# Kernel tuning notes

Hardware: AMD Instinct MI355X
Metric: run time of the kernel (lower is better)

## Reference

```python
import jax, jax.numpy as jnp
import numpy as np

BS, M, CLIP_DIM = 64, 1000, 512
D = 512
N_WAYS = 20
N_Z = 8


def setup_inputs() -> dict:
    key = jax.random.key(0)
    ks = jax.random.split(key, 16)
    s = 0.02
    inp = {
        "x_context": jax.random.normal(ks[0], (BS, M, CLIP_DIM), jnp.float32),
        "y_context": jax.random.randint(ks[1], (BS, M), 0, N_WAYS),
        "x_query": jax.random.normal(ks[2], (BS, M, CLIP_DIM), jnp.float32),
        # image_proj
        "Wp": jax.random.normal(ks[3], (CLIP_DIM, D), jnp.float32) * s,
        "bp": jnp.zeros((D,), jnp.float32),
        # aggregator: Linear(d,d) -> GELU -> Linear(d,2d)
        "Wa1": jax.random.normal(ks[4], (D, D), jnp.float32) * s,
        "ba1": jnp.zeros((D,), jnp.float32),
        "Wa2": jax.random.normal(ks[5], (D, 2 * D), jnp.float32) * s,
        "ba2": jnp.zeros((2 * D,), jnp.float32),
        # decoder: Linear(d,d) -> GELU -> Linear(d,d)
        "Wd1": jax.random.normal(ks[6], (D, D), jnp.float32) * s,
        "bd1": jnp.zeros((D,), jnp.float32),
        "Wd2": jax.random.normal(ks[7], (D, D), jnp.float32) * s,
        "bd2": jnp.zeros((D,), jnp.float32),
    }
    return inp


def reference(x_context, y_context, x_query, Wp, bp, Wa1, ba1, Wa2, ba2, Wd1, bd1, Wd2, bd2):
    # project image embeddings: [bs, M, clip_dim] -> [bs, M, d]
    xc = x_context @ Wp + bp
    xq = x_query @ Wp + bp

    # encode_context_per_class: per-class masked sum == one-hot segment-sum
    # (original loops over classes doing (x*mask).sum(dim=1))
    oh = jax.nn.one_hot(y_context, N_WAYS, dtype=xc.dtype)  # [bs, M, N]
    r_C = jnp.einsum('bmn,bmd->bnd', oh, xc)  # [bs, N, d]

    # knowledge is None -> k = zeros; combined = relu(r + 0)
    combined = jax.nn.relu(r_C)
    h = jax.nn.gelu(combined @ Wa1 + ba1, approximate=False)
    stats = h @ Wa2 + ba2  # [bs, N, 2d]
    mu, scale_raw = stats[..., :D], stats[..., D:]
    scale = 0.01 + 0.99 * jax.nn.softplus(scale_raw)

    # eval path: sample n_z from q(z|C) via reparameterization
    eps = jax.random.normal(jax.random.key(42), (N_Z,) + mu.shape, mu.dtype)
    z_samples = mu[None] + scale[None] * eps  # [n_z, bs, N, d]

    # decode: class weight vectors then inner product with queries
    W = jax.nn.gelu(z_samples @ Wd1 + bd1, approximate=False) @ Wd2 + bd2
    logits = jnp.einsum('bqd,sbnd->sbqn', xq, W)  # [n_z, bs, Q*N, N]
    return logits, z_samples, mu, scale
```

## Files before the change

kernel.cpp:

```cpp
#include <hip/hip_runtime.h>
#include <hip/hip_bf16.h>
#include <stdint.h>


typedef __attribute__((ext_vector_type(8))) short short8;
typedef __attribute__((ext_vector_type(4))) float f32x4;

__device__ __forceinline__ float gelu_f(float x) {
    return 0.5f * x * (1.0f + erff(x * 0.70710678118654752440f));
}
__device__ __forceinline__ float softplus_f(float x) {
    return fmaxf(x, 0.0f) + log1pf(expf(-fabsf(x)));
}
__device__ __forceinline__ uint32_t cvt2(float a, float b) {
    __hip_bfloat162 h;
    h.x = __float2bfloat16(a);
    h.y = __float2bfloat16(b);
    uint32_t u; __builtin_memcpy(&u, &h, 4); return u;
}
__device__ __forceinline__ unsigned short f2bfu(float f) {
    __hip_bfloat16 h = __float2bfloat16(f);
    unsigned short u; __builtin_memcpy(&u, &h, 2); return u;
}
__device__ __forceinline__ float bfu2f(unsigned short u) {
    uint32_t v = (uint32_t)u << 16; float f; __builtin_memcpy(&f, &v, 4); return f;
}

__device__ __forceinline__ void threefry2x32(uint32_t k0, uint32_t k1,
                                             uint32_t x0, uint32_t x1,
                                             uint32_t& o0, uint32_t& o1) {
    uint32_t ks[3] = {k0, k1, k0 ^ k1 ^ 0x1BD11BDAu};
    x0 += ks[0]; x1 += ks[1];
    const uint32_t rot[8] = {13,15,26,6,17,29,16,24};
#pragma unroll
    for (int i = 0; i < 5; i++) {
#pragma unroll
        for (int j = 0; j < 4; j++) {
            uint32_t r = rot[(i & 1) * 4 + j];
            x0 += x1;
            x1 = (x1 << r) | (x1 >> (32 - r));
            x1 ^= x0;
        }
        x0 += ks[(i + 1) % 3];
        x1 += ks[(i + 2) % 3] + (uint32_t)(i + 1);
    }
    o0 = x0; o1 = x1;
}

__device__ __forceinline__ float bits_to_normal(uint32_t b) {
    float f = __uint_as_float((b >> 9) | 0x3F800000u) - 1.0f;
    const float lo = __uint_as_float(0xBF7FFFFFu);
    float u = fmaxf(lo, f * 2.0f + lo);
    return 1.41421356237309504880f * erfinvf(u);
}

__global__ __launch_bounds__(512) void scatter_k(const float* __restrict__ xc,
                                                 const int* __restrict__ y,
                                                 float* __restrict__ Apart,
                                                 float* __restrict__ cntpart) {
    __shared__ float sA[20 * 512];
    __shared__ float scnt[20];
    const int b = blockIdx.x, ch = blockIdx.y;
    const int tid = threadIdx.x;
    for (int i = tid; i < 20 * 512; i += 512) sA[i] = 0.f;
    if (tid < 20) scnt[tid] = 0.f;
    __syncthreads();
    const int m0 = ch * 125;
    const size_t xbase = ((size_t)b * 1000 + m0) * 512 + tid;
    const int ybase = b * 1000 + m0;

    float xv[8]; int cv[8];
#pragma unroll
    for (int j = 0; j < 8; j++) {
        xv[j] = xc[xbase + (size_t)j * 512];
        cv[j] = y[ybase + j];
    }
    int p = 8;
    for (int pan = 0; pan < 15; pan++) {
        float xn[8]; int cn[8];
        const bool more = (pan < 14);
        if (more) {
#pragma unroll
            for (int j = 0; j < 8; j++) {
                xn[j] = xc[xbase + (size_t)(p + j) * 512];
                cn[j] = y[ybase + p + j];
            }
        }
#pragma unroll
        for (int j = 0; j < 8; j++) {
            sA[cv[j] * 512 + tid] += xv[j];
            if (tid == 0) scnt[cv[j]] += 1.f;
        }
        if (more) {
#pragma unroll
            for (int j = 0; j < 8; j++) { xv[j] = xn[j]; cv[j] = cn[j]; }
            p += 8;
        }
    }
#pragma unroll
    for (int j = 0; j < 5; j++) {
        float xx = xc[xbase + (size_t)(120 + j) * 512];
        int cc = y[ybase + 120 + j];
        sA[cc * 512 + tid] += xx;
        if (tid == 0) scnt[cc] += 1.f;
    }
    __syncthreads();
    float* dst = Apart + (size_t)ch * 655360 + (size_t)b * 10240;
    for (int i = tid; i < 10240; i += 512) dst[i] = sA[i];
    if (tid < 20) cntpart[(size_t)ch * 1280 + b * 20 + tid] = scnt[tid];
}

__global__ __launch_bounds__(256) void reduce_bf_k(const float* __restrict__ Apart,
                                                   const float* __restrict__ cntpart,
                                                   unsigned short* __restrict__ Abf,
                                                   float* __restrict__ cnt) {
    int i = blockIdx.x * 256 + threadIdx.x;
    if (i < 163840) {
        const float4* Ap4 = (const float4*)Apart;
        float4 s = Ap4[i];
#pragma unroll
        for (int p = 1; p < 8; p++) {
            float4 v = Ap4[(size_t)p * 163840 + i];
            s.x += v.x; s.y += v.y; s.z += v.z; s.w += v.w;
        }
        uint2 o;
        o.x = cvt2(s.x, s.y); o.y = cvt2(s.z, s.w);
        *(uint2*)&Abf[(size_t)i * 4] = o;
    }
    if (i < 1280) {
        float s = 0.f;
#pragma unroll
        for (int p = 0; p < 8; p++) s += cntpart[p * 1280 + i];
        cnt[i] = s;
    }
}

__global__ __launch_bounds__(256) void wtg_k(const float* __restrict__ src,
                                             unsigned short* __restrict__ dst,
                                             int R, int C) {
    __shared__ float T[64][65];
    const int r0 = blockIdx.y * 64, c0 = blockIdx.x * 64;
    const int tid = threadIdx.x;
    const int rr = tid >> 4, cc = (tid & 15) * 4;
#pragma unroll
    for (int l = 0; l < 4; l++) {
        int row = rr + l * 16;
        float4 v = *(const float4*)&src[(size_t)(r0 + row) * C + c0 + cc];
        T[row][cc] = v.x; T[row][cc+1] = v.y; T[row][cc+2] = v.z; T[row][cc+3] = v.w;
    }
    __syncthreads();
#pragma unroll
    for (int l = 0; l < 4; l++) {
        int n = rr + l * 16;
        uint2 u;
        u.x = cvt2(T[cc][n], T[cc+1][n]);
        u.y = cvt2(T[cc+2][n], T[cc+3][n]);
        *(uint2*)&dst[(size_t)(c0 + n) * R + r0 + cc] = u;
    }
}

__global__ __launch_bounds__(256) void wconv_k(const float* __restrict__ in,
                                               unsigned short* __restrict__ o, int n2) {
    int i = blockIdx.x * 256 + threadIdx.x;
    if (i < n2) {
        float2 v = *(const float2*)&in[i * 2];
        *(uint32_t*)&o[i * 2] = cvt2(v.x, v.y);
    }
}

template <int EPI>
__global__ __launch_bounds__(256) void gm2_k(const unsigned short* __restrict__ Abf,
                                             const unsigned short* __restrict__ Bbf,
                                             const float* __restrict__ bias,
                                             const float* __restrict__ extra,
                                             unsigned short* __restrict__ C0,
                                             float* __restrict__ F0,
                                             float* __restrict__ F1,
                                             int Nn) {
    __shared__ unsigned short As[64 * 64];
    __shared__ unsigned short Bs[128 * 64];
    const int tid = threadIdx.x;
    const int lane = tid & 63, w = tid >> 6;
    const int row0 = blockIdx.y * 64, col0 = blockIdx.x * 128;
    f32x4 acc[4][2] = {};
    for (int k0 = 0; k0 < 512; k0 += 64) {
        {
            int row = tid >> 2, cs = (tid & 3) * 16;
            int swz = (row & 7) << 4;
            const unsigned short* src = Abf + (size_t)(row0 + row) * 512 + k0 + cs;
#pragma unroll
            for (int j = 0; j < 2; j++) {
                uint4 u = *(const uint4*)(src + j * 8);
                *(uint4*)((char*)As + row * 128 + (((cs + j * 8) * 2) ^ swz)) = u;
            }
        }
        {
            int row = tid >> 1, cs = (tid & 1) * 32;
            int swz = (row & 7) << 4;
            const unsigned short* src = Bbf + (size_t)(col0 + row) * 512 + k0 + cs;
#pragma unroll
            for (int j = 0; j < 4; j++) {
                uint4 u = *(const uint4*)(src + j * 8);
                *(uint4*)((char*)Bs + row * 128 + (((cs + j * 8) * 2) ^ swz)) = u;
            }
        }
        __syncthreads();
#pragma unroll
        for (int ks = 0; ks < 2; ks++) {
            short8 a[4], bb[2];
#pragma unroll
            for (int mi = 0; mi < 4; mi++) {
                int r = mi * 16 + (lane & 15);
                a[mi] = *(const short8*)((const char*)As + r * 128 +
                          (((ks * 32 + (lane >> 4) * 8) * 2) ^ ((r & 7) << 4)));
            }
#pragma unroll
            for (int ni = 0; ni < 2; ni++) {
                int n = w * 32 + ni * 16 + (lane & 15);
                bb[ni] = *(const short8*)((const char*)Bs + n * 128 +
                          (((ks * 32 + (lane >> 4) * 8) * 2) ^ ((n & 7) << 4)));
            }
#pragma unroll
            for (int mi = 0; mi < 4; mi++)
#pragma unroll
                for (int ni = 0; ni < 2; ni++)
                    acc[mi][ni] = __builtin_amdgcn_mfma_f32_16x16x32_bf16(a[mi], bb[ni], acc[mi][ni], 0, 0, 0);
        }
        __syncthreads();
    }
#pragma unroll
    for (int mi = 0; mi < 4; mi++) {
#pragma unroll
        for (int ni = 0; ni < 2; ni++) {
            int c = col0 + w * 32 + ni * 16 + (lane & 15);
            float bv = bias ? bias[c] : 0.f;
#pragma unroll
            for (int j = 0; j < 4; j++) {
                int r = row0 + mi * 16 + (lane >> 4) * 4 + j;
                float v = acc[mi][ni][j];
                if (EPI == 0) {
                    v += bv;
                    C0[(size_t)r * Nn + c] = f2bfu(v);
                } else if (EPI == 1) {
                    v += extra[r] * bv;
                    C0[(size_t)r * Nn + c] = f2bfu(fmaxf(v, 0.f));
                } else if (EPI == 2) {
                    C0[(size_t)r * Nn + c] = f2bfu(gelu_f(v + bv));
                } else {
                    v += bv;
                    if (c < 512) F0[(size_t)r * 512 + c] = v;
                    else F1[(size_t)r * 512 + (c - 512)] = 0.01f + 0.99f * softplus_f(v);
                }
            }
        }
    }
}

__global__ __launch_bounds__(256) void z2_k(const float* __restrict__ mu,
                                            const float* __restrict__ sc,
                                            float* __restrict__ z,
                                            unsigned short* __restrict__ zb) {
    const uint32_t NH = 2621440u;
    uint32_t i = blockIdx.x * 256u + threadIdx.x;
    if (i >= NH) return;
    uint32_t t0 = 2u * i;
    uint32_t o0, o1, p0, p1;
    threefry2x32(0u, 42u, 0u, t0, o0, o1);
    threefry2x32(0u, 42u, 0u, t0 + 1u, p0, p1);
    uint32_t r0 = t0 % 655360u;
    float2 mv = *(const float2*)&mu[r0];
    float2 sv = *(const float2*)&sc[r0];
    float z0 = mv.x + sv.x * bits_to_normal(o0 ^ o1);
    float z1 = mv.y + sv.y * bits_to_normal(p0 ^ p1);
    float2 zo; zo.x = z0; zo.y = z1;
    *(float2*)&z[t0] = zo;
    *(uint32_t*)&zb[t0] = cvt2(z0, z1);
}

__global__ __launch_bounds__(256) void beta_bf_k(const unsigned short* __restrict__ Wfb,
                                                 const float* __restrict__ bp,
                                                 float* __restrict__ beta) {
    int wave = threadIdx.x >> 6, lane = threadIdx.x & 63;
    int r = blockIdx.x * 4 + wave;
    short8 wv = *(const short8*)(Wfb + (size_t)r * 512 + lane * 8);
    float s = 0.f;
#pragma unroll
    for (int e = 0; e < 8; e++) s += bp[lane * 8 + e] * bfu2f((unsigned short)wv[e]);
#pragma unroll
    for (int o = 32; o > 0; o >>= 1) s += __shfl_down(s, o, 64);
    if (lane == 0) beta[r] = s;
}

__global__ __launch_bounds__(512) void logits_mfma3_k(const float* __restrict__ Xq,
                                                      const unsigned short* __restrict__ Vb,
                                                      const float* __restrict__ beta,
                                                      float* __restrict__ out) {
    __shared__ unsigned short Vs[160 * 64];
    __shared__ float bs[160];
    const int u = blockIdx.x + 8 * blockIdx.y;
    const int xcd = u & 7, idx = u >> 3;
    const int b = (idx & 7) * 8 + xcd;
    const int qh = idx >> 3;
    const int tid = threadIdx.x, lane = tid & 63, w = tid >> 6;
    const int wq = w >> 1, wn = w & 1;

    if (tid < 160) {
        int s = tid / 20, n = tid - s * 20;
        bs[tid] = beta[(size_t)(s * 64 + b) * 20 + n];
    }

    const int klane = (lane >> 4) * 8;
    const float* xp[2];
    int qb[2];
#pragma unroll
    for (int qs = 0; qs < 2; qs++) {
        qb[qs] = qh * 128 + wq * 32 + qs * 16;
        int qr = qb[qs] + (lane & 15);
        if (qr > 999) qr = 999;
        xp[qs] = Xq + ((size_t)b * 1000 + qr) * 512 + klane;
    }
    int vrow[5], vswz[5];
#pragma unroll
    for (int nf = 0; nf < 5; nf++) {
        int rr = wn * 80 + nf * 16 + (lane & 15);
        vrow[nf] = rr * 128;
        vswz[nf] = (rr & 7) << 4;
    }

    f32x4 acc[2][5] = {};
    for (int k0 = 0; k0 < 512; k0 += 64) {
        __syncthreads();
        for (int c = tid; c < 640; c += 512) {
            int row = c >> 2, off = (c & 3) * 32;
            int sdiv = row / 20;
            int row_g = row + sdiv * 1260 + b * 20;
            const unsigned short* src = Vb + (size_t)row_g * 512 + k0 + (c & 3) * 16;
            uint4 u0 = *(const uint4*)src;
            uint4 u1 = *(const uint4*)(src + 8);
            int swz = (row & 7) << 4;
            char* base = (char*)Vs + row * 128;
            *(uint4*)(base + (off ^ swz)) = u0;
            *(uint4*)(base + ((off + 16) ^ swz)) = u1;
        }
        __syncthreads();
#pragma unroll
        for (int ks = 0; ks < 2; ks++) {
            int kb = (ks * 32 + klane) * 2;
            short8 bf[5];
#pragma unroll
            for (int nf = 0; nf < 5; nf++)
                bf[nf] = *(const short8*)((const char*)Vs + vrow[nf] + (kb ^ vswz[nf]));
            short8 af[2];
#pragma unroll
            for (int qs = 0; qs < 2; qs++) {
                const float* p = xp[qs] + k0 + ks * 32;
                float4 v0 = *(const float4*)p;
                float4 v1 = *(const float4*)(p + 4);
                uint4 uu;
                uu.x = cvt2(v0.x, v0.y); uu.y = cvt2(v0.z, v0.w);
                uu.z = cvt2(v1.x, v1.y); uu.w = cvt2(v1.z, v1.w);
                __builtin_memcpy(&af[qs], &uu, 16);
            }
#pragma unroll
            for (int qs = 0; qs < 2; qs++)
#pragma unroll
                for (int nf = 0; nf < 5; nf++)
                    acc[qs][nf] = __builtin_amdgcn_mfma_f32_16x16x32_bf16(af[qs], bf[nf], acc[qs][nf], 0, 0, 0);
        }
    }

#pragma unroll
    for (int nf = 0; nf < 5; nf++) {
        int rl = wn * 80 + nf * 16 + (lane & 15);
        int s = rl / 20, n = rl - s * 20;
        float bb = bs[rl];
        size_t ob = (size_t)(s * 64 + b) * 20000;
#pragma unroll
        for (int qs = 0; qs < 2; qs++) {
#pragma unroll
            for (int j = 0; j < 4; j++) {
                int q = qb[qs] + (lane >> 4) * 4 + j;
                if (q < 1000)
                    out[ob + (size_t)q * 20 + n] = acc[qs][nf][j] + bb;
            }
        }
    }
}

extern "C" void kernel_launch(void* const* d_in, const int* in_sizes, int n_in,
                              void* d_out, int out_size, void* d_ws, size_t ws_size,
                              hipStream_t stream) {
    const float* x_context = (const float*)d_in[0];
    const int*   y_context = (const int*)d_in[1];
    const float* x_query   = (const float*)d_in[2];
    const float* Wp  = (const float*)d_in[3];
    const float* bp  = (const float*)d_in[4];
    const float* Wa1 = (const float*)d_in[5];
    const float* ba1 = (const float*)d_in[6];
    const float* Wa2 = (const float*)d_in[7];
    const float* ba2 = (const float*)d_in[8];
    const float* Wd1 = (const float*)d_in[9];
    const float* bd1 = (const float*)d_in[10];
    const float* Wd2 = (const float*)d_in[11];
    const float* bd2 = (const float*)d_in[12];

    float* out    = (float*)d_out;
    float* logits = out;
    float* z      = out + 10240000;
    float* mu     = out + 15482880;
    float* sc     = out + 16138240;
    unsigned short* Wfb = (unsigned short*)d_out;

    float* ws   = (float*)d_ws;
    float* cnt  = ws;
    float* beta = cnt + 1280;
    unsigned short* WpTb  = (unsigned short*)(beta + 10240);
    unsigned short* Wa1Tb = WpTb + 262144;
    unsigned short* Wa2Tb = Wa1Tb + 262144;
    unsigned short* WdT1b = Wa2Tb + 524288;
    unsigned short* WdT2b = WdT1b + 262144;
    unsigned short* Wpb   = WdT2b + 262144;
    unsigned short* Abf   = Wpb + 262144;
    unsigned short* combb = Abf + 655360;
    unsigned short* hb    = combb + 655360;
    unsigned short* zb    = hb + 655360;
    unsigned short* Vbf   = zb + 5242880;
    float* big = (float*)(Vbf + 5242880);
    unsigned short* Wgb = (unsigned short*)big;

    wtg_k<<<dim3(8, 8), 256, 0, stream>>>(Wp,  WpTb,  512, 512);
    wtg_k<<<dim3(8, 8), 256, 0, stream>>>(Wa1, Wa1Tb, 512, 512);
    wtg_k<<<dim3(16, 8), 256, 0, stream>>>(Wa2, Wa2Tb, 512, 1024);
    wtg_k<<<dim3(8, 8), 256, 0, stream>>>(Wd1, WdT1b, 512, 512);
    wtg_k<<<dim3(8, 8), 256, 0, stream>>>(Wd2, WdT2b, 512, 512);
    wconv_k<<<dim3(512), 256, 0, stream>>>(Wp, Wpb, 131072);
    scatter_k<<<dim3(64, 8), 512, 0, stream>>>(x_context, y_context, big , beta );
    reduce_bf_k<<<dim3(640), 256, 0, stream>>>(big, beta, Abf, cnt);
    gm2_k<1><<<dim3(4, 20), 256, 0, stream>>>(Abf, WpTb, bp, cnt, combb, nullptr, nullptr, 512);
    gm2_k<2><<<dim3(4, 20), 256, 0, stream>>>(combb, Wa1Tb, ba1, nullptr, hb, nullptr, nullptr, 512);
    gm2_k<3><<<dim3(8, 20), 256, 0, stream>>>(hb, Wa2Tb, ba2, nullptr, nullptr, mu, sc, 1024);
    z2_k<<<dim3(10240), 256, 0, stream>>>(mu, sc, z, zb);
    gm2_k<2><<<dim3(4, 160), 256, 0, stream>>>(zb, WdT1b, bd1, nullptr, Wgb, nullptr, nullptr, 512);
    gm2_k<0><<<dim3(4, 160), 256, 0, stream>>>(Wgb, WdT2b, bd2, nullptr, Wfb, nullptr, nullptr, 512);
    gm2_k<0><<<dim3(4, 160), 256, 0, stream>>>(Wfb, Wpb, nullptr, nullptr, Vbf, nullptr, nullptr, 512);
    beta_bf_k<<<dim3(2560), 256, 0, stream>>>(Wfb, bp, beta);
    logits_mfma3_k<<<dim3(8, 64), 512, 0, stream>>>(x_query, Vbf, beta, logits);
}
```

Baseline: 235.2 us.

## Precompose Wd2 with Wp and fuse weight prep into one kernel

Reassociates the decoder output and image projection by precomputing the product of Wp and Wd2 once as a small GEMM. This removes one large 10240x512x512 GEMM over the sampled weights, and the bias terms are folded into precomputed vectors and a constant. All weight transposes and conversions, the bias dot products and the class counts are merged into a single prep kernel, which cuts launch count; the counts are now computed with shared atomics instead of inside scatter. The composed weight is rounded to bf16, which changes rounding behaviour.

New measurement: 229.4 us. 1.03x faster.

```diff
diff --git a/kernel.cpp b/kernel.cpp
--- a/kernel.cpp
+++ b/kernel.cpp
@@ -54,16 +54,100 @@
     return 1.41421356237309504880f * erfinvf(u);
 }
 
+__global__ __launch_bounds__(256) void prep_k(
+    const float* __restrict__ Wp, const float* __restrict__ Wa1,
+    const float* __restrict__ Wa2, const float* __restrict__ Wd1,
+    const float* __restrict__ Wd2, const float* __restrict__ bp,
+    const float* __restrict__ bd2, const int* __restrict__ y,
+    unsigned short* __restrict__ WpTb, unsigned short* __restrict__ Wa1Tb,
+    unsigned short* __restrict__ Wa2Tb, unsigned short* __restrict__ WdT1b,
+    unsigned short* __restrict__ Wpb, unsigned short* __restrict__ Wd2b,
+    float* __restrict__ bv, float* __restrict__ w2bp,
+    float* __restrict__ c0, float* __restrict__ cnt)
+{
+    __shared__ float T[64][65];
+    __shared__ int lc[32];
+    __shared__ float ws4[4];
+    const int f = blockIdx.x;
+    const int tid = threadIdx.x;
+
+    if (f < 320) {
+        const float* src; unsigned short* dst; int C, t, xb, yb;
+        if (f < 64)       { src = Wp;  dst = WpTb;  C = 512;  t = f;       xb = t & 7;  yb = t >> 3; }
+        else if (f < 128) { src = Wa1; dst = Wa1Tb; C = 512;  t = f - 64;  xb = t & 7;  yb = t >> 3; }
+        else if (f < 256) { src = Wa2; dst = Wa2Tb; C = 1024; t = f - 128; xb = t & 15; yb = t >> 4; }
+        else              { src = Wd1; dst = WdT1b; C = 512;  t = f - 256; xb = t & 7;  yb = t >> 3; }
+        const int r0 = yb * 64, cc0 = xb * 64;
+        const int rr = tid >> 4, cc = (tid & 15) * 4;
+#pragma unroll
+        for (int l = 0; l < 4; l++) {
+            int row = rr + l * 16;
+            float4 v = *(const float4*)&src[(size_t)(r0 + row) * C + cc0 + cc];
+            T[row][cc] = v.x; T[row][cc+1] = v.y; T[row][cc+2] = v.z; T[row][cc+3] = v.w;
+        }
+        __syncthreads();
+#pragma unroll
+        for (int l = 0; l < 4; l++) {
+            int n = rr + l * 16;
+            uint2 u;
+            u.x = cvt2(T[cc][n], T[cc+1][n]);
+            u.y = cvt2(T[cc+2][n], T[cc+3][n]);
+            *(uint2*)&dst[(size_t)(cc0 + n) * 512 + r0 + cc] = u;
+        }
+    } else if (f < 576) {
+        const float* src = (f < 448) ? Wp : Wd2;
+        unsigned short* dst = (f < 448) ? Wpb : Wd2b;
+        int t = (f < 448) ? f - 320 : f - 448;
+        size_t i = ((size_t)t * 256 + tid) * 8;
+        float4 a = *(const float4*)&src[i];
+        float4 b4 = *(const float4*)&src[i + 4];
+        uint4 u;
+        u.x = cvt2(a.x, a.y);  u.y = cvt2(a.z, a.w);
+        u.z = cvt2(b4.x, b4.y); u.w = cvt2(b4.z, b4.w);
+        *(uint4*)&dst[i] = u;
+    } else if (f < 832) {
+        const float* W = (f < 704) ? Wp : Wd2;
+        const float* v = (f < 704) ? bd2 : bp;
+        float* o = (f < 704) ? bv : w2bp;
+        int t = (f < 704) ? f - 576 : f - 704;
+        int wave = tid >> 6, lane = tid & 63;
+        int r = t * 4 + wave;
+        const float* row = W + (size_t)r * 512 + lane * 8;
+        float4 x0 = *(const float4*)row;
+        float4 x1 = *(const float4*)(row + 4);
+        float4 v0 = *(const float4*)&v[lane * 8];
+        float4 v1 = *(const float4*)&v[lane * 8 + 4];
+        float s = x0.x*v0.x + x0.y*v0.y + x0.z*v0.z + x0.w*v0.w
+                + x1.x*v1.x + x1.y*v1.y + x1.z*v1.z + x1.w*v1.w;
+#pragma unroll
+        for (int off = 32; off > 0; off >>= 1) s += __shfl_down(s, off, 64);
+        if (lane == 0) o[r] = s;
+    } else if (f == 832) {
+        float s = bp[tid] * bd2[tid] + bp[tid + 256] * bd2[tid + 256];
+#pragma unroll
+        for (int off = 32; off > 0; off >>= 1) s += __shfl_down(s, off, 64);
+        int wave = tid >> 6, lane = tid & 63;
+        if (lane == 0) ws4[wave] = s;
+        __syncthreads();
+        if (tid == 0) c0[0] = ws4[0] + ws4[1] + ws4[2] + ws4[3];
+    } else {
+        int b = f - 833;
+        if (tid < 32) lc[tid] = 0;
+        __syncthreads();
+        for (int m = tid; m < 1000; m += 256)
+            atomicAdd(&lc[y[b * 1000 + m]], 1);
+        __syncthreads();
+        if (tid < 20) cnt[b * 20 + tid] = (float)lc[tid];
+    }
+}
+
 __global__ __launch_bounds__(512) void scatter_k(const float* __restrict__ xc,
                                                  const int* __restrict__ y,
-                                                 float* __restrict__ Apart,
-                                                 float* __restrict__ cntpart) {
+                                                 float* __restrict__ Apart) {
     __shared__ float sA[20 * 512];
-    __shared__ float scnt[20];
     const int b = blockIdx.x, ch = blockIdx.y;
     const int tid = threadIdx.x;
     for (int i = tid; i < 20 * 512; i += 512) sA[i] = 0.f;
-    if (tid < 20) scnt[tid] = 0.f;
     __syncthreads();
     const int m0 = ch * 125;
     const size_t xbase = ((size_t)b * 1000 + m0) * 512 + tid;
@@ -87,10 +171,7 @@
             }
         }
 #pragma unroll
-        for (int j = 0; j < 8; j++) {
-            sA[cv[j] * 512 + tid] += xv[j];
-            if (tid == 0) scnt[cv[j]] += 1.f;
-        }
+        for (int j = 0; j < 8; j++) sA[cv[j] * 512 + tid] += xv[j];
         if (more) {
 #pragma unroll
             for (int j = 0; j < 8; j++) { xv[j] = xn[j]; cv[j] = cn[j]; }
@@ -102,18 +183,14 @@
         float xx = xc[xbase + (size_t)(120 + j) * 512];
         int cc = y[ybase + 120 + j];
         sA[cc * 512 + tid] += xx;
-        if (tid == 0) scnt[cc] += 1.f;
     }
     __syncthreads();
     float* dst = Apart + (size_t)ch * 655360 + (size_t)b * 10240;
     for (int i = tid; i < 10240; i += 512) dst[i] = sA[i];
-    if (tid < 20) cntpart[(size_t)ch * 1280 + b * 20 + tid] = scnt[tid];
 }
 
 __global__ __launch_bounds__(256) void reduce_bf_k(const float* __restrict__ Apart,
-                                                   const float* __restrict__ cntpart,
-                                                   unsigned short* __restrict__ Abf,
-                                                   float* __restrict__ cnt) {
+                                                   unsigned short* __restrict__ Abf) {
     int i = blockIdx.x * 256 + threadIdx.x;
     if (i < 163840) {
         const float4* Ap4 = (const float4*)Apart;
@@ -126,45 +203,6 @@
         uint2 o;
         o.x = cvt2(s.x, s.y); o.y = cvt2(s.z, s.w);
         *(uint2*)&Abf[(size_t)i * 4] = o;
-    }
-    if (i < 1280) {
-        float s = 0.f;
-#pragma unroll
-        for (int p = 0; p < 8; p++) s += cntpart[p * 1280 + i];
-        cnt[i] = s;
-    }
-}
-
-__global__ __launch_bounds__(256) void wtg_k(const float* __restrict__ src,
-                                             unsigned short* __restrict__ dst,
-                                             int R, int C) {
-    __shared__ float T[64][65];
-    const int r0 = blockIdx.y * 64, c0 = blockIdx.x * 64;
-    const int tid = threadIdx.x;
-    const int rr = tid >> 4, cc = (tid & 15) * 4;
-#pragma unroll
-    for (int l = 0; l < 4; l++) {
-        int row = rr + l * 16;
-        float4 v = *(const float4*)&src[(size_t)(r0 + row) * C + c0 + cc];
-        T[row][cc] = v.x; T[row][cc+1] = v.y; T[row][cc+2] = v.z; T[row][cc+3] = v.w;
-    }
-    __syncthreads();
-#pragma unroll
-    for (int l = 0; l < 4; l++) {
-        int n = rr + l * 16;
-        uint2 u;
-        u.x = cvt2(T[cc][n], T[cc+1][n]);
-        u.y = cvt2(T[cc+2][n], T[cc+3][n]);
-        *(uint2*)&dst[(size_t)(c0 + n) * R + r0 + cc] = u;
-    }
-}
-
-__global__ __launch_bounds__(256) void wconv_k(const float* __restrict__ in,
-                                               unsigned short* __restrict__ o, int n2) {
-    int i = blockIdx.x * 256 + threadIdx.x;
-    if (i < n2) {
-        float2 v = *(const float2*)&in[i * 2];
-        *(uint32_t*)&o[i * 2] = cvt2(v.x, v.y);
     }
 }
 
@@ -277,18 +315,19 @@
     *(uint32_t*)&zb[t0] = cvt2(z0, z1);
 }
 
-__global__ __launch_bounds__(256) void beta_bf_k(const unsigned short* __restrict__ Wfb,
-                                                 const float* __restrict__ bp,
-                                                 float* __restrict__ beta) {
+__global__ __launch_bounds__(256) void beta2_k(const unsigned short* __restrict__ Wgb,
+                                               const float* __restrict__ vec,
+                                               const float* __restrict__ c0,
+                                               float* __restrict__ beta) {
     int wave = threadIdx.x >> 6, lane = threadIdx.x & 63;
     int r = blockIdx.x * 4 + wave;
-    short8 wv = *(const short8*)(Wfb + (size_t)r * 512 + lane * 8);
+    short8 wv = *(const short8*)(Wgb + (size_t)r * 512 + lane * 8);
     float s = 0.f;
 #pragma unroll
-    for (int e = 0; e < 8; e++) s += bp[lane * 8 + e] * bfu2f((unsigned short)wv[e]);
+    for (int e = 0; e < 8; e++) s += vec[lane * 8 + e] * bfu2f((unsigned short)wv[e]);
 #pragma unroll
     for (int o = 32; o > 0; o >>= 1) s += __shfl_down(s, o, 64);
-    if (lane == 0) beta[r] = s;
+    if (lane == 0) beta[r] = s + c0[0];
 }
 
 __global__ __launch_bounds__(512) void logits_mfma3_k(const float* __restrict__ Xq,
@@ -409,18 +448,21 @@
     float* z      = out + 10240000;
     float* mu     = out + 15482880;
     float* sc     = out + 16138240;
-    unsigned short* Wfb = (unsigned short*)d_out;
 
     float* ws   = (float*)d_ws;
     float* cnt  = ws;
     float* beta = cnt + 1280;
-    unsigned short* WpTb  = (unsigned short*)(beta + 10240);
+    float* bv   = beta + 10240;
+    float* w2bp = bv + 512;
+    float* c0   = w2bp + 512;
+    unsigned short* WpTb  = (unsigned short*)(c0 + 63);
     unsigned short* Wa1Tb = WpTb + 262144;
     unsigned short* Wa2Tb = Wa1Tb + 262144;
     unsigned short* WdT1b = Wa2Tb + 524288;
-    unsigned short* WdT2b = WdT1b + 262144;
-    unsigned short* Wpb   = WdT2b + 262144;
-    unsigned short* Abf   = Wpb + 262144;
+    unsigned short* Wpb   = WdT1b + 262144;
+    unsigned short* Wd2b  = Wpb + 262144;
+    unsigned short* Gtb   = Wd2b + 262144;
+    unsigned short* Abf   = Gtb + 262144;
     unsigned short* combb = Abf + 655360;
     unsigned short* hb    = combb + 655360;
     unsigned short* zb    = hb + 655360;
@@ -428,21 +470,18 @@
     float* big = (float*)(Vbf + 5242880);
     unsigned short* Wgb = (unsigned short*)big;
 
-    wtg_k<<<dim3(8, 8), 256, 0, stream>>>(Wp,  WpTb,  512, 512);
-    wtg_k<<<dim3(8, 8), 256, 0, stream>>>(Wa1, Wa1Tb, 512, 512);
-    wtg_k<<<dim3(16, 8), 256, 0, stream>>>(Wa2, Wa2Tb, 512, 1024);
-    wtg_k<<<dim3(8, 8), 256, 0, stream>>>(Wd1, WdT1b, 512, 512);
-    wtg_k<<<dim3(8, 8), 256, 0, stream>>>(Wd2, WdT2b, 512, 512);
-    wconv_k<<<dim3(512), 256, 0, stream>>>(Wp, Wpb, 131072);
-    scatter_k<<<dim3(64, 8), 512, 0, stream>>>(x_context, y_context, big , beta );
-    reduce_bf_k<<<dim3(640), 256, 0, stream>>>(big, beta, Abf, cnt);
+    prep_k<<<dim3(897), 256, 0, stream>>>(Wp, Wa1, Wa2, Wd1, Wd2, bp, bd2, y_context,
+                                          WpTb, Wa1Tb, Wa2Tb, WdT1b, Wpb, Wd2b,
+                                          bv, w2bp, c0, cnt);
+    gm2_k<0><<<dim3(4, 8), 256, 0, stream>>>(Wpb, Wd2b, nullptr, nullptr, Gtb, nullptr, nullptr, 512);
+    scatter_k<<<dim3(64, 8), 512, 0, stream>>>(x_context, y_context, big );
+    reduce_bf_k<<<dim3(640), 256, 0, stream>>>(big, Abf);
     gm2_k<1><<<dim3(4, 20), 256, 0, stream>>>(Abf, WpTb, bp, cnt, combb, nullptr, nullptr, 512);
     gm2_k<2><<<dim3(4, 20), 256, 0, stream>>>(combb, Wa1Tb, ba1, nullptr, hb, nullptr, nullptr, 512);
     gm2_k<3><<<dim3(8, 20), 256, 0, stream>>>(hb, Wa2Tb, ba2, nullptr, nullptr, mu, sc, 1024);
     z2_k<<<dim3(10240), 256, 0, stream>>>(mu, sc, z, zb);
     gm2_k<2><<<dim3(4, 160), 256, 0, stream>>>(zb, WdT1b, bd1, nullptr, Wgb, nullptr, nullptr, 512);
-    gm2_k<0><<<dim3(4, 160), 256, 0, stream>>>(Wgb, WdT2b, bd2, nullptr, Wfb, nullptr, nullptr, 512);
-    gm2_k<0><<<dim3(4, 160), 256, 0, stream>>>(Wfb, Wpb, nullptr, nullptr, Vbf, nullptr, nullptr, 512);
-    beta_bf_k<<<dim3(2560), 256, 0, stream>>>(Wfb, bp, beta);
+    gm2_k<0><<<dim3(4, 160), 256, 0, stream>>>(Wgb, Gtb, bv, nullptr, Vbf, nullptr, nullptr, 512);
+    beta2_k<<<dim3(2560), 256, 0, stream>>>(Wgb, w2bp, c0, beta);
     logits_mfma3_k<<<dim3(8, 64), 512, 0, stream>>>(x_query, Vbf, beta, logits);
 }
```
